# Optimization experiments

Measured on AMD Instinct MI355X. Metric: run time of the kernel, lower is better.

The kernel has to match this reference:

```python
import jax, jax.numpy as jnp
import numpy as np

N, D, H, E = 50000, 512, 8, 3200000
DK = D // H  # 64


def setup_inputs() -> dict:
    key = jax.random.key(0)
    ks = jax.random.split(key, 12)
    x = jax.random.normal(ks[0], (N, D), dtype=jnp.float32)
    row_index = jnp.sort(jax.random.randint(ks[1], (E,), 0, N))
    col_index = jax.random.randint(ks[2], (E,), 0, N)
    att_bias = jax.random.normal(ks[3], (H, E), dtype=jnp.float32)
    # xavier-uniform-ish linear params (bias zero per module init)
    lim = np.sqrt(6.0 / (D + D)).astype(np.float32)
    def w(k):
        return jax.random.uniform(k, (D, D), minval=-lim, maxval=lim, dtype=jnp.float32)
    return {
        "x": x, "row_index": row_index, "col_index": col_index, "att_bias": att_bias,
        "Wq": w(ks[4]), "bq": jnp.zeros((D,), jnp.float32),
        "Wk": w(ks[5]), "bk": jnp.zeros((D,), jnp.float32),
        "Wv": w(ks[6]), "bv": jnp.zeros((D,), jnp.float32),
        "Wo": w(ks[7]), "bo": jnp.zeros((D,), jnp.float32),
    }


def _proj(x, W, b):
    # nn.Linear then reshape(N, H, DK).permute(1,0,2) -> [H, N, DK]
    return (x @ W.T + b).reshape(x.shape[0], H, DK).transpose(1, 0, 2)


def reference(x, row_index, col_index, att_bias, Wq, bq, Wk, bk, Wv, bv, Wo, bo):
    q = _proj(x, Wq, bq) / jnp.sqrt(jnp.float32(DK))  # [H,N,DK]
    k = _proj(x, Wk, bk)
    v = _proj(x, Wv, bv)
    n = x.shape[0]
    # masked QK^T at sparse (row,col) entries + additive sparse bias -> [H,E]
    logits = jnp.einsum("hed,hed->he", q[:, row_index], k[:, col_index]) + att_bias
    # per-row (segment) softmax over CSR rows, vmapped over heads
    seg_max = jax.vmap(lambda l: jax.ops.segment_max(l, row_index, num_segments=n))(logits)  # [H,N]
    p = jnp.exp(logits - seg_max[:, row_index])
    denom = jax.vmap(lambda pe: jax.ops.segment_sum(pe, row_index, num_segments=n))(p)  # [H,N]
    att = p / denom[:, row_index]  # [H,E]
    # sparse att @ V : scatter-add weighted value rows
    y = jax.vmap(lambda a, vc: jax.ops.segment_sum(a[:, None] * vc, row_index, num_segments=n))(
        att, v[:, col_index]
    )  # [H,N,DK]
    y = y.transpose(1, 0, 2).reshape(n, H * DK)  # [N,D]
    return y @ Wo.T + bo
```

## Files before the change

### kernel.cpp

```cpp
#include <hip/hip_runtime.h>
#include <hip/hip_bf16.h>
#include <cstddef>
#include <cstdint>


typedef __attribute__((ext_vector_type(8))) short bf16x8;
typedef __attribute__((ext_vector_type(4))) float f32x4;

#define KQ_SCALE 25.4f
#define KQ_DEQ   0.03937007874f

#if __has_builtin(__builtin_amdgcn_sdot4)
__device__ __forceinline__ int SDOT4(int a, int b, int c) {
    return __builtin_amdgcn_sdot4(a, b, c, false);
}
#else
__device__ __forceinline__ int SDOT4(int a, int b, int c) {
#pragma unroll
    for (int i = 0; i < 4; ++i)
        c += (int)(signed char)((unsigned)a >> (8 * i)) *
             (int)(signed char)((unsigned)b >> (8 * i));
    return c;
}
#endif

__device__ __forceinline__ void gload_lds16(const void* g, const void* l) {
    __builtin_amdgcn_global_load_lds(
        (const __attribute__((address_space(1))) unsigned int*)g,
        (__attribute__((address_space(3))) unsigned int*)l, 16, 0, 0);
}

__device__ __forceinline__ float bflo(unsigned u) { return __uint_as_float(u << 16); }
__device__ __forceinline__ float bfhi(unsigned u) { return __uint_as_float(u & 0xffff0000u); }
__device__ __forceinline__ float ub(unsigned u, int i) {
    return (float)((u >> (i * 8)) & 0xffu);
}

__device__ __forceinline__ void storeT(float* p, size_t i, float v) { p[i] = v; }
__device__ __forceinline__ void storeT(__hip_bfloat16* p, size_t i, float v) {
    p[i] = __float2bfloat16(v);
}
__device__ __forceinline__ void storeT(unsigned char* p, size_t i, float v) {
    const float q = fmaf(v, KQ_SCALE, 128.0f);
    p[i] = (unsigned char)__float2uint_rn(fminf(fmaxf(q, 0.f), 255.f));
}
__device__ __forceinline__ void storeT(signed char* p, size_t i, float v) {
    p[i] = (signed char)__float2int_rn(fminf(fmaxf(v, -127.f), 127.f));
}

__global__ __launch_bounds__(256) void conv_f32_bf16(
    const float* __restrict__ s, __hip_bfloat16* __restrict__ d, int n) {
    const int i = (blockIdx.x * 256 + threadIdx.x) * 8;
    if (i >= n) return;
    const float4 a = *(const float4*)(s + i);
    const float4 b = *(const float4*)(s + i + 4);
    alignas(16) __hip_bfloat16 o[8] = {
        __float2bfloat16(a.x), __float2bfloat16(a.y),
        __float2bfloat16(a.z), __float2bfloat16(a.w),
        __float2bfloat16(b.x), __float2bfloat16(b.y),
        __float2bfloat16(b.z), __float2bfloat16(b.w)};
    *(uint4*)(d + i) = *(const uint4*)o;
}

__global__ void row_start_kernel(const int* __restrict__ row_index,
                                 int* __restrict__ row_start, int n_rows, int E) {
    const int n = blockIdx.x * blockDim.x + threadIdx.x;
    if (n > n_rows) return;
    int lo = 0, hi = E;
    while (lo < hi) {
        const int mid = (lo + hi) >> 1;
        if (row_index[mid] < n) lo = mid + 1; else hi = mid;
    }
    row_start[n] = lo;
}


template <typename TO>
__global__ __launch_bounds__(256) void gemm_mfma_kernel(
    const short* __restrict__ A, const short* __restrict__ Bw,
    const float* __restrict__ bias, TO* __restrict__ C, int M, float scale) {
    __shared__ short As[128 * 32];
    __shared__ short Bs[128 * 32];
    const int t = threadIdx.x;
    const int w = t >> 6, l = t & 63;
    const int m0 = blockIdx.x * 128, n0 = blockIdx.y * 128;
    const int wrow = (w >> 1) * 64, wcol = (w & 1) * 64;
    const int fr = l & 15, fq = l >> 4;

    const int r0 = (w * 64 + l) >> 2, ko0 = ((w * 64 + l) & 3) * 8;
    int gmA0 = m0 + r0;      if (gmA0 >= M) gmA0 = M - 1;
    int gmA1 = m0 + r0 + 64; if (gmA1 >= M) gmA1 = M - 1;
    const int gnB0 = n0 + r0, gnB1 = n0 + r0 + 64;

    f32x4 acc[4][4];
#pragma unroll
    for (int mi = 0; mi < 4; ++mi)
#pragma unroll
        for (int ni = 0; ni < 4; ++ni) acc[mi][ni] = (f32x4){0.f, 0.f, 0.f, 0.f};

    for (int k0 = 0; k0 < 512; k0 += 32) {
        __syncthreads();
        gload_lds16(A + (size_t)gmA0 * 512 + k0 + ko0, As + w * 512);
        gload_lds16(A + (size_t)gmA1 * 512 + k0 + ko0, As + 2048 + w * 512);
        gload_lds16(Bw + (size_t)gnB0 * 512 + k0 + ko0, Bs + w * 512);
        gload_lds16(Bw + (size_t)gnB1 * 512 + k0 + ko0, Bs + 2048 + w * 512);
        __syncthreads();

        bf16x8 af[4], bfr[4];
#pragma unroll
        for (int mi = 0; mi < 4; ++mi)
            af[mi] = *(const bf16x8*)(As + (wrow + mi * 16 + fr) * 32 + fq * 8);
#pragma unroll
        for (int ni = 0; ni < 4; ++ni)
            bfr[ni] = *(const bf16x8*)(Bs + (wcol + ni * 16 + fr) * 32 + fq * 8);
#pragma unroll
        for (int mi = 0; mi < 4; ++mi)
#pragma unroll
            for (int ni = 0; ni < 4; ++ni)
                acc[mi][ni] = __builtin_amdgcn_mfma_f32_16x16x32_bf16(
                    af[mi], bfr[ni], acc[mi][ni], 0, 0, 0);
    }

#pragma unroll
    for (int mi = 0; mi < 4; ++mi)
#pragma unroll
        for (int ni = 0; ni < 4; ++ni)
#pragma unroll
            for (int r = 0; r < 4; ++r) {
                const int gr = m0 + wrow + mi * 16 + fq * 4 + r;
                if (gr < M) {
                    const int gc = n0 + wcol + ni * 16 + fr;
                    storeT(C, (size_t)gr * 512 + gc, (acc[mi][ni][r] + bias[gc]) * scale);
                }
            }
}

__global__ __launch_bounds__(256) void gemm_mfma_quantq_kernel(
    const short* __restrict__ A, const short* __restrict__ Bw,
    const float* __restrict__ bias, signed char* __restrict__ qi8,
    float* __restrict__ qdeq, int M, float scale) {
    __shared__ short As[128 * 32];
    __shared__ short Bs[128 * 32];
    const int t = threadIdx.x;
    const int w = t >> 6, l = t & 63;
    const int m0 = blockIdx.x * 128, n0 = blockIdx.y * 128;
    const int wrow = (w >> 1) * 64, wcol = (w & 1) * 64;
    const int fr = l & 15, fq = l >> 4;

    const int r0 = (w * 64 + l) >> 2, ko0 = ((w * 64 + l) & 3) * 8;
    int gmA0 = m0 + r0;      if (gmA0 >= M) gmA0 = M - 1;
    int gmA1 = m0 + r0 + 64; if (gmA1 >= M) gmA1 = M - 1;
    const int gnB0 = n0 + r0, gnB1 = n0 + r0 + 64;

    f32x4 acc[4][4];
#pragma unroll
    for (int mi = 0; mi < 4; ++mi)
#pragma unroll
        for (int ni = 0; ni < 4; ++ni) acc[mi][ni] = (f32x4){0.f, 0.f, 0.f, 0.f};

    for (int k0 = 0; k0 < 512; k0 += 32) {
        __syncthreads();
        gload_lds16(A + (size_t)gmA0 * 512 + k0 + ko0, As + w * 512);
        gload_lds16(A + (size_t)gmA1 * 512 + k0 + ko0, As + 2048 + w * 512);
        gload_lds16(Bw + (size_t)gnB0 * 512 + k0 + ko0, Bs + w * 512);
        gload_lds16(Bw + (size_t)gnB1 * 512 + k0 + ko0, Bs + 2048 + w * 512);
        __syncthreads();

        bf16x8 af[4], bfr[4];
#pragma unroll
        for (int mi = 0; mi < 4; ++mi)
            af[mi] = *(const bf16x8*)(As + (wrow + mi * 16 + fr) * 32 + fq * 8);
#pragma unroll
        for (int ni = 0; ni < 4; ++ni)
            bfr[ni] = *(const bf16x8*)(Bs + (wcol + ni * 16 + fr) * 32 + fq * 8);
#pragma unroll
        for (int mi = 0; mi < 4; ++mi)
#pragma unroll
            for (int ni = 0; ni < 4; ++ni)
                acc[mi][ni] = __builtin_amdgcn_mfma_f32_16x16x32_bf16(
                    af[mi], bfr[ni], acc[mi][ni], 0, 0, 0);
    }

    const int head = (n0 + wcol) >> 6;
#pragma unroll
    for (int mi = 0; mi < 4; ++mi)
#pragma unroll
        for (int r = 0; r < 4; ++r) {
            const int gr = m0 + wrow + mi * 16 + fq * 4 + r;
            float v[4];
            float a = 0.f;
#pragma unroll
            for (int ni = 0; ni < 4; ++ni) {
                const int gc = n0 + wcol + ni * 16 + fr;
                v[ni] = (acc[mi][ni][r] + bias[gc]) * scale;
                a = fmaxf(a, fabsf(v[ni]));
            }
#pragma unroll
            for (int st = 1; st < 16; st <<= 1) a = fmaxf(a, __shfl_xor(a, st, 64));
            const float sc = (a > 0.f) ? 127.0f / a : 0.f;
            if (gr < M) {
#pragma unroll
                for (int ni = 0; ni < 4; ++ni) {
                    const int gc = n0 + wcol + ni * 16 + fr;
                    qi8[(size_t)gr * 512 + gc] =
                        (signed char)__float2int_rn(v[ni] * sc);
                }
                if (fr == 0) qdeq[(size_t)gr * 8 + head] = a * (1.0f / 127.0f);
            }
        }
}

__global__ __launch_bounds__(256) void sparse_attn_kernel(
    const signed char* __restrict__ qi8, const float* __restrict__ qdeq,
    const signed char* __restrict__ kq, const unsigned char* __restrict__ vq,
    const int* __restrict__ col_index, const float* __restrict__ att_bias,
    const int* __restrict__ row_start, __hip_bfloat16* __restrict__ yout, int E) {
    const int n = blockIdx.x;
    const int w = threadIdx.x >> 6;
    const int lane = threadIdx.x & 63;
    const int g = lane & 7;
    const int j = lane >> 3;
    const int hA = 2 * w + (g >> 2);
    const int dim0 = (g & 3) * 16;
    const int e0 = row_start[n], e1 = row_start[n + 1];

    const int4 qu = *(const int4*)(qi8 + (size_t)n * 512 + hA * 64 + dim0);
    const float dsc = qdeq[(size_t)n * 8 + hA] * KQ_DEQ;

    const float* biasH = att_bias + (size_t)hA * (size_t)E;
    const unsigned pairoff = (unsigned)(w * 128 + g * 16);

    float acc[16];
#pragma unroll
    for (int i = 0; i < 16; ++i) acc[i] = 0.f;
    float s_lane = 0.f;

    if (e0 < e1) {
        const int e1m1 = e1 - 1;
        for (int base = e0; base < e1; base += 32) {
            int ec[4]; unsigned co[4];
#pragma unroll
            for (int t = 0; t < 4; ++t) {
                ec[t] = min(base + t * 8 + j, e1m1);
                co[t] = ((unsigned)col_index[ec[t]] << 9) + pairoff;
            }
            int4 ku[4]; uint4 vu[4]; float bv[4];
#pragma unroll
            for (int t = 0; t < 4; ++t) {
                ku[t] = *(const int4*)(kq + co[t]);
                vu[t] = *(const uint4*)(vq + co[t]);
                bv[t] = biasH[ec[t]];
            }

            int id[4];
#pragma unroll
            for (int t = 0; t < 4; ++t) {
                int a0 = 0, a1 = 0;
                a0 = SDOT4(qu.x, ku[t].x, a0);
                a1 = SDOT4(qu.y, ku[t].y, a1);
                a0 = SDOT4(qu.z, ku[t].z, a0);
                a1 = SDOT4(qu.w, ku[t].w, a1);
                id[t] = a0 + a1;
            }
#pragma unroll
            for (int t = 0; t < 4; ++t) {
                id[t] += __shfl_xor(id[t], 1, 64);
                id[t] += __shfl_xor(id[t], 2, 64);
            }
            float p[4];
#pragma unroll
            for (int t = 0; t < 4; ++t)
                p[t] = (base + t * 8 + j < e1)
                           ? __expf(fmaf((float)id[t], dsc, bv[t]))
                           : 0.f;
            s_lane += (p[0] + p[1]) + (p[2] + p[3]);

#pragma unroll
            for (int t = 0; t < 4; ++t) {
                const unsigned* u = (const unsigned*)&vu[t];
#pragma unroll
                for (int i = 0; i < 4; ++i)
#pragma unroll
                    for (int b = 0; b < 4; ++b)
                        acc[4 * i + b] = fmaf(p[t], ub(u[i], b), acc[4 * i + b]);
            }
        }
    }

#pragma unroll
    for (int st = 8; st < 64; st <<= 1) s_lane += __shfl_xor(s_lane, st, 64);
#pragma unroll
    for (int i = 0; i < 16; ++i) {
#pragma unroll
        for (int st = 8; st < 64; st <<= 1) acc[i] += __shfl_xor(acc[i], st, 64);
    }

    float y0 = acc[0], y1 = acc[1];
#pragma unroll
    for (int t = 1; t < 8; ++t) {
        y0 = (j == t) ? acc[2 * t] : y0;
        y1 = (j == t) ? acc[2 * t + 1] : y1;
    }
    const size_t orow = (size_t)n * 512 + hA * 64 + dim0 + 2 * j;
    if (s_lane > 0.f) {
        const float inv = 1.0f / s_lane;
        yout[orow]     = __float2bfloat16(fmaf(KQ_DEQ, y0 * inv, -128.0f * KQ_DEQ));
        yout[orow + 1] = __float2bfloat16(fmaf(KQ_DEQ, y1 * inv, -128.0f * KQ_DEQ));
    } else {
        yout[orow]     = __float2bfloat16(0.f);
        yout[orow + 1] = __float2bfloat16(0.f);
    }
}

extern "C" void kernel_launch(void* const* d_in, const int* in_sizes, int n_in,
                              void* d_out, int out_size, void* d_ws, size_t ws_size,
                              hipStream_t stream) {
    const float* x         = (const float*)d_in[0];
    const int*   row_index = (const int*)d_in[1];
    const int*   col_index = (const int*)d_in[2];
    const float* att_bias  = (const float*)d_in[3];
    const float* Wq = (const float*)d_in[4];
    const float* bq = (const float*)d_in[5];
    const float* Wk = (const float*)d_in[6];
    const float* bk = (const float*)d_in[7];
    const float* Wv = (const float*)d_in[8];
    const float* bv = (const float*)d_in[9];
    const float* Wo = (const float*)d_in[10];
    const float* bo = (const float*)d_in[11];
    float* out = (float*)d_out;

    const int N = in_sizes[0] / 512;
    const int E = in_sizes[1];
    const int WN = 512 * 512;

    char* ws = (char*)d_ws;
    const size_t nb = (size_t)N * 512 * sizeof(__hip_bfloat16);
    const size_t b8 = (size_t)N * 512;
    const size_t wb = (size_t)WN * sizeof(__hip_bfloat16);
    __hip_bfloat16* xb  = (__hip_bfloat16*)(ws);
    signed char*    kq8 = (signed char*)(ws + nb);
    unsigned char*  vq8 = (unsigned char*)(ws + nb + b8);
    signed char*    qi8 = (signed char*)(ws + nb + 2 * b8);
    __hip_bfloat16* wqb = (__hip_bfloat16*)(ws + nb + 3 * b8);
    __hip_bfloat16* wkb = (__hip_bfloat16*)(ws + nb + 3 * b8 + wb);
    __hip_bfloat16* wvb = (__hip_bfloat16*)(ws + nb + 3 * b8 + 2 * wb);
    __hip_bfloat16* wob = (__hip_bfloat16*)(ws + nb + 3 * b8 + 3 * wb);
    float* qdeq = (float*)(ws + nb + 3 * b8 + 4 * wb);
    int* row_start = (int*)(ws + nb + 3 * b8 + 4 * wb + (size_t)N * 8 * 4);

    conv_f32_bf16<<<(N * 512 / 8 + 255) / 256, 256, 0, stream>>>(x, xb, N * 512);
    conv_f32_bf16<<<(WN / 8 + 255) / 256, 256, 0, stream>>>(Wq, wqb, WN);
    conv_f32_bf16<<<(WN / 8 + 255) / 256, 256, 0, stream>>>(Wk, wkb, WN);
    conv_f32_bf16<<<(WN / 8 + 255) / 256, 256, 0, stream>>>(Wv, wvb, WN);
    conv_f32_bf16<<<(WN / 8 + 255) / 256, 256, 0, stream>>>(Wo, wob, WN);

    row_start_kernel<<<(N + 1 + 255) / 256, 256, 0, stream>>>(row_index, row_start, N, E);

    const dim3 gg((N + 127) / 128, 4), gb(256);
    gemm_mfma_quantq_kernel<<<gg, gb, 0, stream>>>(
        (const short*)xb, (const short*)wqb, bq, qi8, qdeq, N, 0.125f);
    gemm_mfma_kernel<signed char><<<gg, gb, 0, stream>>>(
        (const short*)xb, (const short*)wkb, bk, kq8, N, KQ_SCALE);
    gemm_mfma_kernel<unsigned char><<<gg, gb, 0, stream>>>(
        (const short*)xb, (const short*)wvb, bv, vq8, N, 1.0f);

    sparse_attn_kernel<<<N, 256, 0, stream>>>(
        qi8, qdeq, kq8, vq8, col_index, att_bias, row_start, xb , E);

    gemm_mfma_kernel<float><<<gg, gb, 0, stream>>>(
        (const short*)xb, (const short*)wob, bo, out, N, 1.0f);
}
```

Before: 757.3 us.

## Enlarge GEMM tiles to 128x256 with 512-thread blocks sharing A tile

The projection GEMMs now use 128x256 output tiles with 8 waves per block instead of 128x128 tiles with 4 waves, so each A (activation) tile loaded into LDS is reused across twice as many output columns. The shared main loop is factored into a helper used by both the plain and the quantizing GEMM, and the grid drops to 2 column blocks. This cuts redundant global loads of x but halves the number of blocks and doubles LDS per block, which may lower occupancy or wave scheduling flexibility.

```diff
diff --git a/kernel.cpp b/kernel.cpp
--- a/kernel.cpp
+++ b/kernel.cpp
@@ -74,52 +74,61 @@
     row_start[n] = lo;
 }
 
+__device__ __forceinline__ void gemm_core_128x256(
+    const short* __restrict__ A, const short* __restrict__ Bw, int M,
+    short* As, short* Bs, f32x4 (&acc)[4][4]) {
+    const int t = threadIdx.x;
+    const int w = t >> 6, l = t & 63;
+    const int m0 = blockIdx.x * 128, n0 = blockIdx.y * 256;
+    const int wrow = (w & 1) * 64, wcol = (w >> 1) * 64;
+    const int fr = l & 15, fq = l >> 4;
+    const int rA = t >> 2, koA = (t & 3) * 8;
+    int gmA = m0 + rA; if (gmA >= M) gmA = M - 1;
+    const int gnB0 = n0 + rA, gnB1 = n0 + 128 + rA;
+    const int dstA = t * 8;
+
+#pragma unroll
+    for (int mi = 0; mi < 4; ++mi)
+#pragma unroll
+        for (int ni = 0; ni < 4; ++ni) acc[mi][ni] = (f32x4){0.f, 0.f, 0.f, 0.f};
+
+    for (int k0 = 0; k0 < 512; k0 += 32) {
+        __syncthreads();
+        gload_lds16(A + (size_t)gmA * 512 + k0 + koA, As + dstA);
+        gload_lds16(Bw + (size_t)gnB0 * 512 + k0 + koA, Bs + dstA);
+        gload_lds16(Bw + (size_t)gnB1 * 512 + k0 + koA, Bs + 4096 + dstA);
+        __syncthreads();
+
+        bf16x8 af[4], bfr[4];
+#pragma unroll
+        for (int mi = 0; mi < 4; ++mi)
+            af[mi] = *(const bf16x8*)(As + (wrow + mi * 16 + fr) * 32 + fq * 8);
+#pragma unroll
+        for (int ni = 0; ni < 4; ++ni)
+            bfr[ni] = *(const bf16x8*)(Bs + (wcol + ni * 16 + fr) * 32 + fq * 8);
+#pragma unroll
+        for (int mi = 0; mi < 4; ++mi)
+#pragma unroll
+            for (int ni = 0; ni < 4; ++ni)
+                acc[mi][ni] = __builtin_amdgcn_mfma_f32_16x16x32_bf16(
+                    af[mi], bfr[ni], acc[mi][ni], 0, 0, 0);
+    }
+}
 
 template <typename TO>
-__global__ __launch_bounds__(256) void gemm_mfma_kernel(
+__global__ __launch_bounds__(512) void gemm_mfma_kernel(
     const short* __restrict__ A, const short* __restrict__ Bw,
     const float* __restrict__ bias, TO* __restrict__ C, int M, float scale) {
     __shared__ short As[128 * 32];
-    __shared__ short Bs[128 * 32];
+    __shared__ short Bs[256 * 32];
+    f32x4 acc[4][4];
+    gemm_core_128x256(A, Bw, M, As, Bs, acc);
+
     const int t = threadIdx.x;
     const int w = t >> 6, l = t & 63;
-    const int m0 = blockIdx.x * 128, n0 = blockIdx.y * 128;
-    const int wrow = (w >> 1) * 64, wcol = (w & 1) * 64;
+    const int m0 = blockIdx.x * 128, n0 = blockIdx.y * 256;
+    const int wrow = (w & 1) * 64, wcol = (w >> 1) * 64;
     const int fr = l & 15, fq = l >> 4;
-
-    const int r0 = (w * 64 + l) >> 2, ko0 = ((w * 64 + l) & 3) * 8;
-    int gmA0 = m0 + r0;      if (gmA0 >= M) gmA0 = M - 1;
-    int gmA1 = m0 + r0 + 64; if (gmA1 >= M) gmA1 = M - 1;
-    const int gnB0 = n0 + r0, gnB1 = n0 + r0 + 64;
-
-    f32x4 acc[4][4];
-#pragma unroll
-    for (int mi = 0; mi < 4; ++mi)
-#pragma unroll
-        for (int ni = 0; ni < 4; ++ni) acc[mi][ni] = (f32x4){0.f, 0.f, 0.f, 0.f};
-
-    for (int k0 = 0; k0 < 512; k0 += 32) {
-        __syncthreads();
-        gload_lds16(A + (size_t)gmA0 * 512 + k0 + ko0, As + w * 512);
-        gload_lds16(A + (size_t)gmA1 * 512 + k0 + ko0, As + 2048 + w * 512);
-        gload_lds16(Bw + (size_t)gnB0 * 512 + k0 + ko0, Bs + w * 512);
-        gload_lds16(Bw + (size_t)gnB1 * 512 + k0 + ko0, Bs + 2048 + w * 512);
-        __syncthreads();
-
-        bf16x8 af[4], bfr[4];
-#pragma unroll
-        for (int mi = 0; mi < 4; ++mi)
-            af[mi] = *(const bf16x8*)(As + (wrow + mi * 16 + fr) * 32 + fq * 8);
-#pragma unroll
-        for (int ni = 0; ni < 4; ++ni)
-            bfr[ni] = *(const bf16x8*)(Bs + (wcol + ni * 16 + fr) * 32 + fq * 8);
-#pragma unroll
-        for (int mi = 0; mi < 4; ++mi)
-#pragma unroll
-            for (int ni = 0; ni < 4; ++ni)
-                acc[mi][ni] = __builtin_amdgcn_mfma_f32_16x16x32_bf16(
-                    af[mi], bfr[ni], acc[mi][ni], 0, 0, 0);
-    }
 
 #pragma unroll
     for (int mi = 0; mi < 4; ++mi)
@@ -130,58 +139,28 @@
                 const int gr = m0 + wrow + mi * 16 + fq * 4 + r;
                 if (gr < M) {
                     const int gc = n0 + wcol + ni * 16 + fr;
-                    storeT(C, (size_t)gr * 512 + gc, (acc[mi][ni][r] + bias[gc]) * scale);
+                    storeT(C, (size_t)gr * 512 + gc,
+                           (acc[mi][ni][r] + bias[gc]) * scale);
                 }
             }
 }
 
-__global__ __launch_bounds__(256) void gemm_mfma_quantq_kernel(
+__global__ __launch_bounds__(512) void gemm_mfma_quantq_kernel(
     const short* __restrict__ A, const short* __restrict__ Bw,
     const float* __restrict__ bias, signed char* __restrict__ qi8,
     float* __restrict__ qdeq, int M, float scale) {
     __shared__ short As[128 * 32];
-    __shared__ short Bs[128 * 32];
+    __shared__ short Bs[256 * 32];
+    f32x4 acc[4][4];
+    gemm_core_128x256(A, Bw, M, As, Bs, acc);
+
     const int t = threadIdx.x;
     const int w = t >> 6, l = t & 63;
-    const int m0 = blockIdx.x * 128, n0 = blockIdx.y * 128;
-    const int wrow = (w >> 1) * 64, wcol = (w & 1) * 64;
+    const int m0 = blockIdx.x * 128, n0 = blockIdx.y * 256;
+    const int wrow = (w & 1) * 64, wcol = (w >> 1) * 64;
     const int fr = l & 15, fq = l >> 4;
-
-    const int r0 = (w * 64 + l) >> 2, ko0 = ((w * 64 + l) & 3) * 8;
-    int gmA0 = m0 + r0;      if (gmA0 >= M) gmA0 = M - 1;
-    int gmA1 = m0 + r0 + 64; if (gmA1 >= M) gmA1 = M - 1;
-    const int gnB0 = n0 + r0, gnB1 = n0 + r0 + 64;
-
-    f32x4 acc[4][4];
-#pragma unroll
-    for (int mi = 0; mi < 4; ++mi)
-#pragma unroll
-        for (int ni = 0; ni < 4; ++ni) acc[mi][ni] = (f32x4){0.f, 0.f, 0.f, 0.f};
-
-    for (int k0 = 0; k0 < 512; k0 += 32) {
-        __syncthreads();
-        gload_lds16(A + (size_t)gmA0 * 512 + k0 + ko0, As + w * 512);
-        gload_lds16(A + (size_t)gmA1 * 512 + k0 + ko0, As + 2048 + w * 512);
-        gload_lds16(Bw + (size_t)gnB0 * 512 + k0 + ko0, Bs + w * 512);
-        gload_lds16(Bw + (size_t)gnB1 * 512 + k0 + ko0, Bs + 2048 + w * 512);
-        __syncthreads();
-
-        bf16x8 af[4], bfr[4];
-#pragma unroll
-        for (int mi = 0; mi < 4; ++mi)
-            af[mi] = *(const bf16x8*)(As + (wrow + mi * 16 + fr) * 32 + fq * 8);
-#pragma unroll
-        for (int ni = 0; ni < 4; ++ni)
-            bfr[ni] = *(const bf16x8*)(Bs + (wcol + ni * 16 + fr) * 32 + fq * 8);
-#pragma unroll
-        for (int mi = 0; mi < 4; ++mi)
-#pragma unroll
-            for (int ni = 0; ni < 4; ++ni)
-                acc[mi][ni] = __builtin_amdgcn_mfma_f32_16x16x32_bf16(
-                    af[mi], bfr[ni], acc[mi][ni], 0, 0, 0);
-    }
-
     const int head = (n0 + wcol) >> 6;
+
 #pragma unroll
     for (int mi = 0; mi < 4; ++mi)
 #pragma unroll
@@ -196,7 +175,8 @@
                 a = fmaxf(a, fabsf(v[ni]));
             }
 #pragma unroll
-            for (int st = 1; st < 16; st <<= 1) a = fmaxf(a, __shfl_xor(a, st, 64));
+            for (int st = 1; st < 16; st <<= 1)
+                a = fmaxf(a, __shfl_xor(a, st, 64));
             const float sc = (a > 0.f) ? 127.0f / a : 0.f;
             if (gr < M) {
 #pragma unroll
@@ -356,7 +336,7 @@
 
     row_start_kernel<<<(N + 1 + 255) / 256, 256, 0, stream>>>(row_index, row_start, N, E);
 
-    const dim3 gg((N + 127) / 128, 4), gb(256);
+    const dim3 gg((N + 127) / 128, 2), gb(512);
     gemm_mfma_quantq_kernel<<<gg, gb, 0, stream>>>(
         (const short*)xb, (const short*)wqb, bq, qi8, qdeq, N, 0.125f);
     gemm_mfma_kernel<signed char><<<gg, gb, 0, stream>>>(
```

Result: faster. 703.1 us (-7.1%).
